# Kernel tuning notes

Hardware: AMD Instinct MI355X
Metric: run time of the kernel (lower is better)

Reference implementation:

```python
import jax, jax.numpy as jnp
import numpy as np

N, D_IN, D_HID, D_OUT, E = 100000, 128, 256, 64, 1600000


def setup_inputs() -> dict:
    key = jax.random.key(0)
    ks = jax.random.split(key, 6)
    x = jax.random.normal(ks[0], (N, D_IN), dtype=jnp.float32)
    edge_index = jax.random.randint(ks[1], (2, E), 0, N, dtype=jnp.int64)
    # Linear params (PyTorch convention: y = x @ W.T + b)
    W1 = jax.random.normal(ks[2], (D_HID, D_IN), dtype=jnp.float32) / np.sqrt(D_IN)
    b1 = jax.random.normal(ks[3], (D_HID,), dtype=jnp.float32) * 0.01
    W2 = jax.random.normal(ks[4], (D_OUT, D_HID), dtype=jnp.float32) / np.sqrt(D_HID)
    b2 = jax.random.normal(ks[5], (D_OUT,), dtype=jnp.float32) * 0.01
    return {"x": x, "edge_index": edge_index, "W1": W1, "b1": b1, "W2": W2, "b2": b2}


def _scatter_mean(vals, dst, num_nodes):
    # sum neighbor features per destination node, divide by in-degree (0-degree -> 0)
    s = jax.ops.segment_sum(vals, dst, num_segments=num_nodes)
    cnt = jax.ops.segment_sum(jnp.ones((dst.shape[0],), vals.dtype), dst, num_segments=num_nodes)
    return s / jnp.maximum(cnt, 1.0)[:, None]


def _sage_layer(x, src, dst, W, b):
    neighbors = x[src]                      # [E, d] gather
    agg = _scatter_mean(neighbors, dst, x.shape[0])  # [N, d]
    return agg @ W.T + b


def reference(x, edge_index, W1, b1, W2, b2):
    src, dst = edge_index[0], edge_index[1]
    h = _sage_layer(x, src, dst, W1, b1)
    h = jax.nn.relu(h)
    # dropout is identity at inference (training=False)
    y = _sage_layer(h, src, dst, W2, b2)
    return jax.nn.log_softmax(y, axis=1)
```

## Files before the change

kernel.cpp:

```cpp
#include <hip/hip_runtime.h>


typedef __attribute__((ext_vector_type(8))) short bf16x8;
typedef __attribute__((ext_vector_type(4))) float f32x4;
typedef __attribute__((ext_vector_type(2))) float f32x2;

#define BSHIFT 8
#define BMASK  255
#define SRCMASK 0x1FFFF
#define TBIN   4096

#if __has_builtin(__builtin_amdgcn_cvt_pk_f32_fp8) && __has_builtin(__builtin_amdgcn_cvt_pk_fp8_f32)
#define HAVE_FP8_CVT 1
#else
#define HAVE_FP8_CVT 0
#endif

__device__ inline ushort f2bf(float f) {
  union { float f; unsigned u; } c; c.f = f;
  unsigned r = (c.u + 0x7fffu + ((c.u >> 16) & 1u)) >> 16;
  return (ushort)r;
}

#if HAVE_FP8_CVT
template <bool HI>
__device__ inline f32x2 fp8x2f(unsigned w) {
  return __builtin_amdgcn_cvt_pk_f32_fp8((int)w, HI);
}
template <bool HI>
__device__ inline unsigned fp8pack2(unsigned old, float a, float b) {
  return (unsigned)__builtin_amdgcn_cvt_pk_fp8_f32(a, b, (int)old, HI);
}
#else
__device__ inline float fp8tof_1(unsigned b) {
  unsigned e = (b >> 3) & 15u, m = b & 7u;
  float v;
  if (e == 0) v = (float)m * 0x1p-9f;
  else { union { unsigned u; float f; } c; c.u = ((e + 120u) << 23) | (m << 20); v = c.f; }
  return (b & 0x80u) ? -v : v;
}
template <bool HI>
__device__ inline f32x2 fp8x2f(unsigned w) {
  unsigned sh = HI ? 16 : 0;
  f32x2 r;
  r.x = fp8tof_1((w >> sh) & 0xFFu);
  r.y = fp8tof_1((w >> (sh + 8)) & 0xFFu);
  return r;
}
__device__ inline unsigned f2fp8_1(float f) {
  float af = fabsf(f);
  unsigned s = (f < 0.f) ? 0x80u : 0u;
  if (!(af < 448.f)) return s | 0x7Eu;
  if (af < 0x1p-6f) {
    int m = (int)rintf(af * 512.0f);
    if (m >= 8) return s | 0x08u;
    return s | (unsigned)m;
  }
  int e;
  frexpf(af, &e);
  int E = e - 1;
  int q = (int)rintf(ldexpf(af, 3 - E));
  if (q >= 16) { q = 8; E += 1; if (E > 8) return s | 0x7Eu; }
  return s | ((unsigned)(E + 7) << 3) | ((unsigned)q & 7u);
}
template <bool HI>
__device__ inline unsigned fp8pack2(unsigned old, float a, float b) {
  unsigned pair = f2fp8_1(a) | (f2fp8_1(b) << 8);
  return HI ? ((old & 0x0000FFFFu) | (pair << 16)) : ((old & 0xFFFF0000u) | pair);
}
#endif

__global__ void __launch_bounds__(256) k_prep_x(const float4* __restrict__ x4, uint2* __restrict__ xq8, int total8) {
  int i = blockIdx.x * 256 + threadIdx.x;
  if (i >= total8) return;
  float4 v0 = x4[2 * i], v1 = x4[2 * i + 1];
  unsigned w0 = fp8pack2<false>(0u, v0.x, v0.y);
  w0 = fp8pack2<true>(w0, v0.z, v0.w);
  unsigned w1 = fp8pack2<false>(0u, v1.x, v1.y);
  w1 = fp8pack2<true>(w1, v1.z, v1.w);
  xq8[i] = make_uint2(w0, w1);
}

__global__ void __launch_bounds__(256) k_prep_w(const float* __restrict__ W1, const float* __restrict__ W2,
                                                ushort* __restrict__ W1f, ushort* __restrict__ W2f,
                                                const int* __restrict__ ei, int* __restrict__ flag,
                                                unsigned long long* __restrict__ xpad,
                                                unsigned long long* __restrict__ gpad) {
  if (blockIdx.x == 0) {
    int t = threadIdx.x;
    if (t < 64) {
      int v = ei[2 * t + 1];
      unsigned long long m = __ballot(v != 0);
      if (t == 0) *flag = (m == 0ull) ? 1 : 0;
      if (t < 16) xpad[t] = 0ull;
      if (t < 8)  gpad[t] = 0ull;
    }
  }
  int idx = blockIdx.x * 256 + threadIdx.x;
  if (idx < 32768) {
    int jt = idx >> 11, rem = idx & 2047;
    int kt = rem >> 9, rem2 = rem & 511;
    int l = rem2 >> 3, e = rem2 & 7;
    int k = kt * 32 + (l >> 4) * 8 + e;
    int j = jt * 16 + (l & 15);
    W1f[idx] = f2bf(W1[j * 128 + k]);
  } else {
    int i2 = idx - 32768;
    if (i2 < 16384) {
      int ot = i2 >> 12, rem = i2 & 4095;
      int kt = rem >> 9;
      int l = (rem >> 3) & 63, e = rem & 7;
      int k = kt * 32 + (l >> 4) * 8 + e;
      int o = ot * 16 + (l & 15);
      W2f[i2] = f2bf(W2[o * 256 + k]);
    }
  }
}

__global__ void __launch_bounds__(256) k_bhist(const int* __restrict__ ei, const int* __restrict__ flag,
                                               int* __restrict__ bcnt, int E, int NB) {
  __shared__ int h[512];
  int t = threadIdx.x;
  h[t] = 0; h[t + 256] = 0;
  __syncthreads();
  bool f64 = (*flag != 0);
  int stride = gridDim.x * 256;
  for (int e = blockIdx.x * 256 + t; e < E; e += stride) {
    int d;
    if (f64) d = (int)((const long long*)ei)[(size_t)E + e];
    else     d = ei[(size_t)E + e];
    atomicAdd(&h[d >> BSHIFT], 1);
  }
  __syncthreads();
  if (t < NB && h[t]) atomicAdd(&bcnt[t], h[t]);
  int t2 = t + 256;
  if (t2 < NB && h[t2]) atomicAdd(&bcnt[t2], h[t2]);
}

__global__ void __launch_bounds__(512) k_bscan(const int* __restrict__ bcnt, int* __restrict__ bbase,
                                               int* __restrict__ bcur, int* __restrict__ row_ptr,
                                               int NB, int N, int E) {
  __shared__ int s[512];
  int t = threadIdx.x;
  int v = (t < NB) ? bcnt[t] : 0;
  s[t] = v;
  __syncthreads();
  for (int o = 1; o < 512; o <<= 1) {
    int u = (t >= o) ? s[t - o] : 0;
    __syncthreads();
    s[t] += u;
    __syncthreads();
  }
  if (t < NB) {
    int base = s[t] - v;
    bbase[t] = base;
    bcur[t] = base;
  }
  if (t == 0) {
    bbase[NB] = E;
    row_ptr[N] = E;
  }
}

__global__ void __launch_bounds__(256) k_bin(const int* __restrict__ ei, const int* __restrict__ flag,
                                             int* __restrict__ bcur, int* __restrict__ gpair, int E, int NB) {
  __shared__ int hist[512], base[512], segb[512], cur[512], scanb[512];
  __shared__ int ent[TBIN];
  __shared__ int gdx[TBIN];
  int t = threadIdx.x;
  int e0 = blockIdx.x * TBIN;
  int cnt = E - e0; if (cnt > TBIN) cnt = TBIN;
  hist[t] = 0; hist[t + 256] = 0;
  __syncthreads();
  bool f64 = (*flag != 0);
  int ment[16], mbk[16];
#pragma unroll
  for (int i = 0; i < 16; ++i) {
    int idx = t + i * 256;
    mbk[i] = -1;
    if (idx < cnt) {
      int e = e0 + idx;
      int s, d;
      if (f64) {
        const long long* p = (const long long*)ei;
        s = (int)p[e];
        d = (int)p[(size_t)E + e];
      } else {
        s = ei[e];
        d = ei[(size_t)E + e];
      }
      int b = d >> BSHIFT;
      mbk[i] = b;
      ment[i] = ((d & BMASK) << 17) | s;
      atomicAdd(&hist[b], 1);
    }
  }
  __syncthreads();
  scanb[t] = hist[t]; scanb[t + 256] = hist[t + 256];
  __syncthreads();
  for (int o = 1; o < 512; o <<= 1) {
    int u0 = (t >= o) ? scanb[t - o] : 0;
    int t2 = t + 256;
    int u1 = (t2 >= o) ? scanb[t2 - o] : 0;
    __syncthreads();
    scanb[t] += u0; scanb[t + 256] += u1;
    __syncthreads();
  }
  {
    int b0 = scanb[t] - hist[t];
    base[t] = b0;
    cur[t] = b0;
    segb[t] = (t < NB && hist[t] > 0) ? atomicAdd(&bcur[t], hist[t]) : 0;
    int t2 = t + 256;
    int b1 = scanb[t2] - hist[t2];
    base[t2] = b1;
    cur[t2] = b1;
    segb[t2] = (t2 < NB && hist[t2] > 0) ? atomicAdd(&bcur[t2], hist[t2]) : 0;
  }
  __syncthreads();
#pragma unroll
  for (int i = 0; i < 16; ++i) {
    int b = mbk[i];
    if (b >= 0) {
      int pos = atomicAdd(&cur[b], 1);
      ent[pos] = ment[i];
      gdx[pos] = segb[b] + (pos - base[b]);
    }
  }
  __syncthreads();
  for (int i = t; i < cnt; i += 256) gpair[gdx[i]] = ent[i];
}

__global__ void __launch_bounds__(256) k_bcsr(const int* __restrict__ gpair, const int* __restrict__ bbase,
                                              int* __restrict__ row_ptr, float* __restrict__ inv_deg,
                                              int* __restrict__ csr, int N) {
  __shared__ int hist[256], pre[256], cur[256];
  int b = blockIdx.x, t = threadIdx.x;
  int start = bbase[b], end = bbase[b + 1];
  hist[t] = 0;
  __syncthreads();
  for (int i = start + t; i < end; i += 256) {
    int e = gpair[i];
    atomicAdd(&hist[e >> 17], 1);
  }
  __syncthreads();
  pre[t] = hist[t];
  __syncthreads();
  for (int o = 1; o < 256; o <<= 1) {
    int u = (t >= o) ? pre[t - o] : 0;
    __syncthreads();
    pre[t] += u;
    __syncthreads();
  }
  int gbase = start + pre[t] - hist[t];
  int n = (b << BSHIFT) + t;
  if (n < N) {
    row_ptr[n] = gbase;
    inv_deg[n] = 1.0f / (float)(hist[t] > 0 ? hist[t] : 1);
  }
  cur[t] = gbase;
  __syncthreads();
  for (int i = start + t; i < end; i += 256) {
    int e = gpair[i];
    int pos = atomicAdd(&cur[e >> 17], 1);
    csr[pos] = e & SRCMASK;
  }
}

__global__ void __launch_bounds__(256) k_agg1(const unsigned char* __restrict__ xq, const int* __restrict__ csr,
                                              const int* __restrict__ row_ptr, const float* __restrict__ inv_deg,
                                              ushort* __restrict__ agg1b, int N) {
  const int lane = threadIdx.x & 63;
  const int g = lane >> 4;
  const int g16 = lane & 48;
  const int p = lane & 15;
  const int h = (lane >> 3) & 1;
  const int c = lane & 7;
  const unsigned coff = (unsigned)c * 16u;
  const int shbase = g16 + h;

  const int quad = blockIdx.x * 4 + (threadIdx.x >> 6);
  const int n0 = quad * 4;
  if (n0 >= N) return;
  int rp = n0 + (lane < 4 ? lane : 4);
  if (rp > N) rp = N;
  const int rv = row_ptr[rp];
  const int n = n0 + g;
  const int s = __shfl(rv, g);
  const int cnt = __shfl(rv, g + 1) - s;
  int maxc = cnt;
  maxc = max(maxc, __shfl_xor(maxc, 16));
  maxc = max(maxc, __shfl_xor(maxc, 32));

  f32x2 a[8];
#pragma unroll
  for (int i = 0; i < 8; ++i) a[i] = (f32x2)(0.f);

  int ci = (p < cnt) ? csr[s + p] : N;
  for (int base = 0; base < maxc; base += 16) {
    uint4 wv[8];
#pragma unroll
    for (int u = 0; u < 8; ++u) {
      int idx = __shfl(ci, shbase + 2 * u);
      wv[u] = *(const uint4*)(xq + (((unsigned)idx << 7) + coff));
    }
    int li = base + 16 + p;
    int cin = (li < cnt) ? csr[s + li] : N;
#pragma unroll
    for (int u = 0; u < 8; ++u) {
      a[0] += fp8x2f<false>(wv[u].x); a[1] += fp8x2f<true>(wv[u].x);
      a[2] += fp8x2f<false>(wv[u].y); a[3] += fp8x2f<true>(wv[u].y);
      a[4] += fp8x2f<false>(wv[u].z); a[5] += fp8x2f<true>(wv[u].z);
      a[6] += fp8x2f<false>(wv[u].w); a[7] += fp8x2f<true>(wv[u].w);
    }
    ci = cin;
  }
#pragma unroll
  for (int i = 0; i < 8; ++i) {
    a[i].x += __shfl_xor(a[i].x, 8);
    a[i].y += __shfl_xor(a[i].y, 8);
  }
  if (n < N) {
    const float inv = inv_deg[n];
    bf16x8 o;
#pragma unroll
    for (int k = 0; k < 4; ++k) {
      f32x2 v0 = a[k], v1 = a[k + 4];
      float vx = h ? v1.x : v0.x;
      float vy = h ? v1.y : v0.y;
      o[2 * k]     = (short)f2bf(vx * inv);
      o[2 * k + 1] = (short)f2bf(vy * inv);
    }
    *(bf16x8*)(agg1b + (size_t)n * 128 + c * 16 + h * 8) = o;
  }
}

__global__ void __launch_bounds__(256) k_mlp(const ushort* __restrict__ agg1b, const bf16x8* __restrict__ w1f,
                                             const float* __restrict__ b1, const bf16x8* __restrict__ w2f,
                                             unsigned char* __restrict__ gq, int N) {
  __shared__ __align__(16) ushort sm[16896];
  ushort* aT = sm;
  ushort* hT = sm;
  const int t = threadIdx.x;
  const int n0 = blockIdx.x * 64;

#pragma unroll
  for (int i = 0; i < 4; ++i) {
    int idx = i * 256 + t;
    int row = idx >> 4, c8 = idx & 15;
    int rr = n0 + row; if (rr >= N) rr = N - 1;
    bf16x8 v = *(const bf16x8*)(agg1b + (size_t)rr * 128 + c8 * 8);
    *(bf16x8*)(aT + row * 136 + c8 * 8) = v;
  }
  __syncthreads();

  const int w = t >> 6, l = t & 63;
  const int lm = l & 15, lq = l >> 4;

  f32x4 acc[4][4];
#pragma unroll
  for (int mt = 0; mt < 4; ++mt)
#pragma unroll
    for (int nt = 0; nt < 4; ++nt) acc[mt][nt] = (f32x4)(0.f);

#pragma unroll
  for (int kt = 0; kt < 4; ++kt) {
    bf16x8 b[4], a[4];
#pragma unroll
    for (int nt = 0; nt < 4; ++nt)
      b[nt] = w1f[((w * 4 + nt) * 4 + kt) * 64 + l];
#pragma unroll
    for (int mt = 0; mt < 4; ++mt)
      a[mt] = *(const bf16x8*)(aT + (mt * 16 + lm) * 136 + kt * 32 + lq * 8);
#pragma unroll
    for (int mt = 0; mt < 4; ++mt)
#pragma unroll
      for (int nt = 0; nt < 4; ++nt)
        acc[mt][nt] = __builtin_amdgcn_mfma_f32_16x16x32_bf16(a[mt], b[nt], acc[mt][nt], 0, 0, 0);
  }
  __syncthreads();

#pragma unroll
  for (int nt = 0; nt < 4; ++nt) {
    int col = w * 64 + nt * 16 + lm;
    float bb = b1[col];
#pragma unroll
    for (int mt = 0; mt < 4; ++mt)
#pragma unroll
      for (int r = 0; r < 4; ++r) {
        int row = mt * 16 + lq * 4 + r;
        float hv = acc[mt][nt][r] + bb;
        hT[row * 264 + col] = f2bf(fmaxf(hv, 0.f));
      }
  }
  __syncthreads();

  f32x4 acc2[4];
#pragma unroll
  for (int ot = 0; ot < 4; ++ot) acc2[ot] = (f32x4)(0.f);
#pragma unroll
  for (int kt = 0; kt < 8; ++kt) {
    bf16x8 a2 = *(const bf16x8*)(hT + (w * 16 + lm) * 264 + kt * 32 + lq * 8);
#pragma unroll
    for (int ot = 0; ot < 4; ++ot) {
      bf16x8 bf = w2f[(ot * 8 + kt) * 64 + l];
      acc2[ot] = __builtin_amdgcn_mfma_f32_16x16x32_bf16(a2, bf, acc2[ot], 0, 0, 0);
    }
  }
#pragma unroll
  for (int ot = 0; ot < 4; ++ot)
#pragma unroll
    for (int r = 0; r < 4; ++r) {
      int row = n0 + w * 16 + lq * 4 + r;
      if (row < N) {
        unsigned pw = fp8pack2<false>(0u, acc2[ot][r], acc2[ot][r]);
        gq[(size_t)row * 64 + ot * 16 + lm] = (unsigned char)(pw & 0xFFu);
      }
    }
}

__global__ void __launch_bounds__(256) k_agg2(const unsigned char* __restrict__ gq, const int* __restrict__ csr,
                                              const int* __restrict__ row_ptr, const float* __restrict__ inv_deg,
                                              const float* __restrict__ b2, float* __restrict__ out, int N) {
  const int lane = threadIdx.x & 63;
  const int g = lane >> 4;
  const int g16 = lane & 48;
  const int p = lane & 15;
  const int q2 = (lane >> 2) & 3;
  const int c = lane & 3;
  const unsigned coff = (unsigned)c * 16u;
  const int shbase = g16 + q2;

  const int quad = blockIdx.x * 4 + (threadIdx.x >> 6);
  const int n0 = quad * 4;
  if (n0 >= N) return;
  int rp = n0 + (lane < 4 ? lane : 4);
  if (rp > N) rp = N;
  const int rv = row_ptr[rp];
  const int n = n0 + g;
  const int s = __shfl(rv, g);
  const int cnt = __shfl(rv, g + 1) - s;
  int maxc = cnt;
  maxc = max(maxc, __shfl_xor(maxc, 16));
  maxc = max(maxc, __shfl_xor(maxc, 32));

  f32x2 a[8];
#pragma unroll
  for (int i = 0; i < 8; ++i) a[i] = (f32x2)(0.f);

  int ci0 = (p < cnt) ? csr[s + p] : N;
  int li1 = 16 + p;
  int ci1 = (li1 < cnt) ? csr[s + li1] : N;
  for (int base = 0; base < maxc; base += 32) {
    uint4 wv[8];
#pragma unroll
    for (int u = 0; u < 4; ++u) {
      int idx = __shfl(ci0, shbase + 4 * u);
      wv[u] = *(const uint4*)(gq + (((unsigned)idx << 6) + coff));
    }
#pragma unroll
    for (int u = 0; u < 4; ++u) {
      int idx = __shfl(ci1, shbase + 4 * u);
      wv[4 + u] = *(const uint4*)(gq + (((unsigned)idx << 6) + coff));
    }
    int li2 = base + 32 + p, li3 = base + 48 + p;
    int cin0 = (li2 < cnt) ? csr[s + li2] : N;
    int cin1 = (li3 < cnt) ? csr[s + li3] : N;
#pragma unroll
    for (int u = 0; u < 8; ++u) {
      a[0] += fp8x2f<false>(wv[u].x); a[1] += fp8x2f<true>(wv[u].x);
      a[2] += fp8x2f<false>(wv[u].y); a[3] += fp8x2f<true>(wv[u].y);
      a[4] += fp8x2f<false>(wv[u].z); a[5] += fp8x2f<true>(wv[u].z);
      a[6] += fp8x2f<false>(wv[u].w); a[7] += fp8x2f<true>(wv[u].w);
    }
    ci0 = cin0; ci1 = cin1;
  }
#pragma unroll
  for (int i = 0; i < 8; ++i) {
    a[i].x += __shfl_xor(a[i].x, 4); a[i].y += __shfl_xor(a[i].y, 4);
    a[i].x += __shfl_xor(a[i].x, 8); a[i].y += __shfl_xor(a[i].y, 8);
  }
  const float inv = inv_deg[n < N ? n : 0];
  float4 bv0 = *(const float4*)(b2 + c * 16);
  float4 bv1 = *(const float4*)(b2 + c * 16 + 4);
  float4 bv2 = *(const float4*)(b2 + c * 16 + 8);
  float4 bv3 = *(const float4*)(b2 + c * 16 + 12);
  float v[16];
  v[0]  = a[0].x * inv + bv0.x;  v[1]  = a[0].y * inv + bv0.y;
  v[2]  = a[1].x * inv + bv0.z;  v[3]  = a[1].y * inv + bv0.w;
  v[4]  = a[2].x * inv + bv1.x;  v[5]  = a[2].y * inv + bv1.y;
  v[6]  = a[3].x * inv + bv1.z;  v[7]  = a[3].y * inv + bv1.w;
  v[8]  = a[4].x * inv + bv2.x;  v[9]  = a[4].y * inv + bv2.y;
  v[10] = a[5].x * inv + bv2.z;  v[11] = a[5].y * inv + bv2.w;
  v[12] = a[6].x * inv + bv3.x;  v[13] = a[6].y * inv + bv3.y;
  v[14] = a[7].x * inv + bv3.z;  v[15] = a[7].y * inv + bv3.w;
  float mx = v[0];
#pragma unroll
  for (int j = 1; j < 16; ++j) mx = fmaxf(mx, v[j]);
  mx = fmaxf(mx, __shfl_xor(mx, 1));
  mx = fmaxf(mx, __shfl_xor(mx, 2));
  float se = 0.f;
#pragma unroll
  for (int j = 0; j < 16; ++j) se += expf(v[j] - mx);
  se += __shfl_xor(se, 1);
  se += __shfl_xor(se, 2);
  float lse = mx + logf(se);
  if (n < N && q2 == 0) {
    float* po = out + (size_t)n * 64 + c * 16;
    float4 o0, o1, o2, o3;
    o0.x = v[0] - lse;  o0.y = v[1] - lse;  o0.z = v[2] - lse;  o0.w = v[3] - lse;
    o1.x = v[4] - lse;  o1.y = v[5] - lse;  o1.z = v[6] - lse;  o1.w = v[7] - lse;
    o2.x = v[8] - lse;  o2.y = v[9] - lse;  o2.z = v[10] - lse; o2.w = v[11] - lse;
    o3.x = v[12] - lse; o3.y = v[13] - lse; o3.z = v[14] - lse; o3.w = v[15] - lse;
    *(float4*)(po)      = o0;
    *(float4*)(po + 4)  = o1;
    *(float4*)(po + 8)  = o2;
    *(float4*)(po + 12) = o3;
  }
}

extern "C" void kernel_launch(void* const* d_in, const int* in_sizes, int n_in,
                              void* d_out, int out_size, void* d_ws, size_t ws_size,
                              hipStream_t stream) {
  const float* x  = (const float*)d_in[0];
  const int*   ei = (const int*)d_in[1];
  const float* W1 = (const float*)d_in[2];
  const float* b1 = (const float*)d_in[3];
  const float* W2 = (const float*)d_in[4];
  const float* b2 = (const float*)d_in[5];
  float* out = (float*)d_out;
  const int N = in_sizes[0] / 128;
  const int E = in_sizes[1] / 2;
  const int NB = (N + BMASK) >> BSHIFT;

  char* base = (char*)d_ws;
  size_t off = 0;
  auto alloc = [&](size_t bytes) -> char* {
    char* p = base + off;
    off += (bytes + 255) & ~(size_t)255;
    return p;
  };
  int*    flag    = (int*)alloc(4);
  int*    bcnt    = (int*)alloc((size_t)NB * 4);
  int*    bbase   = (int*)alloc((size_t)(NB + 1) * 4);
  int*    bcur    = (int*)alloc((size_t)NB * 4);
  int*    gpair   = (int*)alloc((size_t)E * 4);
  int*    row_ptr = (int*)alloc((size_t)(N + 1) * 4);
  float*  inv_deg = (float*)alloc((size_t)N * 4);
  int*    csr     = (int*)alloc((size_t)E * 4);
  unsigned char* xq = (unsigned char*)alloc((size_t)(N + 1) * 128);
  ushort* W1f     = (ushort*)alloc((size_t)32768 * 2);
  ushort* W2f     = (ushort*)alloc((size_t)16384 * 2);
  ushort* agg1b   = (ushort*)alloc((size_t)N * 128 * 2);
  unsigned char* gq = (unsigned char*)alloc((size_t)(N + 1) * 64);
  (void)ws_size; (void)n_in; (void)out_size;

  hipMemsetAsync(bcnt, 0, (size_t)NB * 4, stream);
  k_prep_x<<<(N * 16 + 255) / 256, 256, 0, stream>>>((const float4*)x, (uint2*)xq, N * 16);
  k_prep_w<<<192, 256, 0, stream>>>(W1, W2, W1f, W2f, ei, flag,
                                    (unsigned long long*)(xq + (size_t)N * 128),
                                    (unsigned long long*)(gq + (size_t)N * 64));
  k_bhist<<<512, 256, 0, stream>>>(ei, flag, bcnt, E, NB);
  k_bscan<<<1, 512, 0, stream>>>(bcnt, bbase, bcur, row_ptr, NB, N, E);
  k_bin<<<(E + TBIN - 1) / TBIN, 256, 0, stream>>>(ei, flag, bcur, gpair, E, NB);
  k_bcsr<<<NB, 256, 0, stream>>>(gpair, bbase, row_ptr, inv_deg, csr, N);
  k_agg1<<<(N + 15) / 16, 256, 0, stream>>>(xq, csr, row_ptr, inv_deg, agg1b, N);
  k_mlp<<<(N + 63) / 64, 256, 0, stream>>>(agg1b, (const bf16x8*)W1f, b1, (const bf16x8*)W2f, gq, N);
  k_agg2<<<(N + 15) / 16, 256, 0, stream>>>(gq, csr, row_ptr, inv_deg, b2, out, N);
}
```

Measured before the change: 246.0 us.

## Fuse prep, histogram and scan into one front kernel with last-block scan

Result: slower. 259.5 us (+5.5%).

```diff
diff --git a/kernel.cpp b/kernel.cpp
--- a/kernel.cpp
+++ b/kernel.cpp
@@ -9,6 +9,7 @@
 #define BMASK  255
 #define SRCMASK 0x1FFFF
 #define TBIN   4096
+#define NHB    512
 
 #if __has_builtin(__builtin_amdgcn_cvt_pk_f32_fp8) && __has_builtin(__builtin_amdgcn_cvt_pk_fp8_f32)
 #define HAVE_FP8_CVT 1
@@ -70,95 +71,99 @@
 }
 #endif
 
-__global__ void __launch_bounds__(256) k_prep_x(const float4* __restrict__ x4, uint2* __restrict__ xq8, int total8) {
-  int i = blockIdx.x * 256 + threadIdx.x;
-  if (i >= total8) return;
-  float4 v0 = x4[2 * i], v1 = x4[2 * i + 1];
-  unsigned w0 = fp8pack2<false>(0u, v0.x, v0.y);
-  w0 = fp8pack2<true>(w0, v0.z, v0.w);
-  unsigned w1 = fp8pack2<false>(0u, v1.x, v1.y);
-  w1 = fp8pack2<true>(w1, v1.z, v1.w);
-  xq8[i] = make_uint2(w0, w1);
-}
-
-__global__ void __launch_bounds__(256) k_prep_w(const float* __restrict__ W1, const float* __restrict__ W2,
-                                                ushort* __restrict__ W1f, ushort* __restrict__ W2f,
-                                                const int* __restrict__ ei, int* __restrict__ flag,
-                                                unsigned long long* __restrict__ xpad,
-                                                unsigned long long* __restrict__ gpad) {
-  if (blockIdx.x == 0) {
-    int t = threadIdx.x;
+__global__ void __launch_bounds__(256) k_front(const float4* __restrict__ x4, uint2* __restrict__ xq8, int total8,
+                                               const float* __restrict__ W1, const float* __restrict__ W2,
+                                               ushort* __restrict__ W1f, ushort* __restrict__ W2f,
+                                               const int* __restrict__ ei, int* __restrict__ flag,
+                                               unsigned long long* __restrict__ xpad,
+                                               unsigned long long* __restrict__ gpad,
+                                               int* __restrict__ bcnt, int* __restrict__ done,
+                                               int* __restrict__ bbase, int* __restrict__ bcur,
+                                               int* __restrict__ row_ptr,
+                                               int E, int NB, int N) {
+  const int bid = blockIdx.x;
+  const int t = threadIdx.x;
+  if (bid < NHB) {
+    __shared__ int h[512];
+    __shared__ int sf64, ticket;
+    h[t] = 0; h[t + 256] = 0;
     if (t < 64) {
+      int v = ei[2 * t + 1];
+      unsigned long long m = __ballot(v != 0);
+      if (t == 0) sf64 = (m == 0ull) ? 1 : 0;
+    }
+    __syncthreads();
+    const bool f64 = (sf64 != 0);
+    const int stride = NHB * 256;
+    for (int e = bid * 256 + t; e < E; e += stride) {
+      int d;
+      if (f64) d = (int)((const long long*)ei)[(size_t)E + e];
+      else     d = ei[(size_t)E + e];
+      atomicAdd(&h[d >> BSHIFT], 1);
+    }
+    __syncthreads();
+    const int t2 = t + 256;
+    if (t < NB && h[t]) atomicAdd(&bcnt[t], h[t]);
+    if (t2 < NB && h[t2]) atomicAdd(&bcnt[t2], h[t2]);
+    __threadfence();
+    __syncthreads();
+    if (t == 0) ticket = atomicAdd(done, 1);
+    __syncthreads();
+    if (ticket == NHB - 1) {
+      __shared__ int s[512];
+      int v0 = (t < NB) ? atomicAdd(&bcnt[t], 0) : 0;
+      int v1 = (t2 < NB) ? atomicAdd(&bcnt[t2], 0) : 0;
+      s[t] = v0; s[t2] = v1;
+      __syncthreads();
+      for (int o = 1; o < 512; o <<= 1) {
+        int u0 = (t >= o) ? s[t - o] : 0;
+        int u1 = (t2 >= o) ? s[t2 - o] : 0;
+        __syncthreads();
+        s[t] += u0; s[t2] += u1;
+        __syncthreads();
+      }
+      if (t < NB) { int b0 = s[t] - v0; bbase[t] = b0; bcur[t] = b0; }
+      if (t2 < NB) { int b1 = s[t2] - v1; bbase[t2] = b1; bcur[t2] = b1; }
+      if (t == 0) { bbase[NB] = E; row_ptr[N] = E; }
+    }
+  } else if (bid < NHB + 192) {
+    const int wb = bid - NHB;
+    if (wb == 0 && t < 64) {
       int v = ei[2 * t + 1];
       unsigned long long m = __ballot(v != 0);
       if (t == 0) *flag = (m == 0ull) ? 1 : 0;
       if (t < 16) xpad[t] = 0ull;
       if (t < 8)  gpad[t] = 0ull;
     }
-  }
-  int idx = blockIdx.x * 256 + threadIdx.x;
-  if (idx < 32768) {
-    int jt = idx >> 11, rem = idx & 2047;
-    int kt = rem >> 9, rem2 = rem & 511;
-    int l = rem2 >> 3, e = rem2 & 7;
-    int k = kt * 32 + (l >> 4) * 8 + e;
-    int j = jt * 16 + (l & 15);
-    W1f[idx] = f2bf(W1[j * 128 + k]);
+    int idx = wb * 256 + t;
+    if (idx < 32768) {
+      int jt = idx >> 11, rem = idx & 2047;
+      int kt = rem >> 9, rem2 = rem & 511;
+      int l = rem2 >> 3, e = rem2 & 7;
+      int k = kt * 32 + (l >> 4) * 8 + e;
+      int j = jt * 16 + (l & 15);
+      W1f[idx] = f2bf(W1[j * 128 + k]);
+    } else {
+      int i2 = idx - 32768;
+      if (i2 < 16384) {
+        int ot = i2 >> 12, rem = i2 & 4095;
+        int kt = rem >> 9;
+        int l = (rem >> 3) & 63, e = rem & 7;
+        int k = kt * 32 + (l >> 4) * 8 + e;
+        int o = ot * 16 + (l & 15);
+        W2f[i2] = f2bf(W2[o * 256 + k]);
+      }
+    }
   } else {
-    int i2 = idx - 32768;
-    if (i2 < 16384) {
-      int ot = i2 >> 12, rem = i2 & 4095;
-      int kt = rem >> 9;
-      int l = (rem >> 3) & 63, e = rem & 7;
-      int k = kt * 32 + (l >> 4) * 8 + e;
-      int o = ot * 16 + (l & 15);
-      W2f[i2] = f2bf(W2[o * 256 + k]);
-    }
-  }
-}
-
-__global__ void __launch_bounds__(256) k_bhist(const int* __restrict__ ei, const int* __restrict__ flag,
-                                               int* __restrict__ bcnt, int E, int NB) {
-  __shared__ int h[512];
-  int t = threadIdx.x;
-  h[t] = 0; h[t + 256] = 0;
-  __syncthreads();
-  bool f64 = (*flag != 0);
-  int stride = gridDim.x * 256;
-  for (int e = blockIdx.x * 256 + t; e < E; e += stride) {
-    int d;
-    if (f64) d = (int)((const long long*)ei)[(size_t)E + e];
-    else     d = ei[(size_t)E + e];
-    atomicAdd(&h[d >> BSHIFT], 1);
-  }
-  __syncthreads();
-  if (t < NB && h[t]) atomicAdd(&bcnt[t], h[t]);
-  int t2 = t + 256;
-  if (t2 < NB && h[t2]) atomicAdd(&bcnt[t2], h[t2]);
-}
-
-__global__ void __launch_bounds__(512) k_bscan(const int* __restrict__ bcnt, int* __restrict__ bbase,
-                                               int* __restrict__ bcur, int* __restrict__ row_ptr,
-                                               int NB, int N, int E) {
-  __shared__ int s[512];
-  int t = threadIdx.x;
-  int v = (t < NB) ? bcnt[t] : 0;
-  s[t] = v;
-  __syncthreads();
-  for (int o = 1; o < 512; o <<= 1) {
-    int u = (t >= o) ? s[t - o] : 0;
-    __syncthreads();
-    s[t] += u;
-    __syncthreads();
-  }
-  if (t < NB) {
-    int base = s[t] - v;
-    bbase[t] = base;
-    bcur[t] = base;
-  }
-  if (t == 0) {
-    bbase[NB] = E;
-    row_ptr[N] = E;
+    int i = (bid - NHB - 192) * 256 + t;
+    if (i < total8) {
+      float4 v0 = x4[2 * i], v1 = x4[2 * i + 1];
+      unsigned w0 = fp8pack2<false>(0u, v0.x, v0.y);
+      w0 = fp8pack2<true>(w0, v0.z, v0.w);
+      unsigned w1 = fp8pack2<false>(0u, v1.x, v1.y);
+      w1 = fp8pack2<true>(w1, v1.z, v1.w);
+      xq8[i] = make_uint2(w0, w1);
+    }
   }
 }
 
@@ -541,7 +546,7 @@
     return p;
   };
   int*    flag    = (int*)alloc(4);
-  int*    bcnt    = (int*)alloc((size_t)NB * 4);
+  int*    bcnt    = (int*)alloc((size_t)(NB + 1) * 4);
   int*    bbase   = (int*)alloc((size_t)(NB + 1) * 4);
   int*    bcur    = (int*)alloc((size_t)NB * 4);
   int*    gpair   = (int*)alloc((size_t)E * 4);
@@ -555,13 +560,16 @@
   unsigned char* gq = (unsigned char*)alloc((size_t)(N + 1) * 64);
   (void)ws_size; (void)n_in; (void)out_size;
 
-  hipMemsetAsync(bcnt, 0, (size_t)NB * 4, stream);
-  k_prep_x<<<(N * 16 + 255) / 256, 256, 0, stream>>>((const float4*)x, (uint2*)xq, N * 16);
-  k_prep_w<<<192, 256, 0, stream>>>(W1, W2, W1f, W2f, ei, flag,
-                                    (unsigned long long*)(xq + (size_t)N * 128),
-                                    (unsigned long long*)(gq + (size_t)N * 64));
-  k_bhist<<<512, 256, 0, stream>>>(ei, flag, bcnt, E, NB);
-  k_bscan<<<1, 512, 0, stream>>>(bcnt, bbase, bcur, row_ptr, NB, N, E);
+  const int total8 = N * 16;
+  const int NPX = (total8 + 255) / 256;
+
+  hipMemsetAsync(bcnt, 0, (size_t)(NB + 1) * 4, stream);
+  k_front<<<NHB + 192 + NPX, 256, 0, stream>>>((const float4*)x, (uint2*)xq, total8,
+                                               W1, W2, W1f, W2f, ei, flag,
+                                               (unsigned long long*)(xq + (size_t)N * 128),
+                                               (unsigned long long*)(gq + (size_t)N * 64),
+                                               bcnt, bcnt + NB, bbase, bcur, row_ptr,
+                                               E, NB, N);
   k_bin<<<(E + TBIN - 1) / TBIN, 256, 0, stream>>>(ei, flag, bcur, gpair, E, NB);
   k_bcsr<<<NB, 256, 0, stream>>>(gpair, bbase, row_ptr, inv_deg, csr, N);
   k_agg1<<<(N + 15) / 16, 256, 0, stream>>>(xq, csr, row_ptr, inv_deg, agg1b, N);
```

## Fuse first-layer neighbor aggregation into the MLP kernel via shared memory

Applied to the files above, without the earlier changes.

Result: slower. 263.3 us (+7.0%).

```diff
diff --git a/kernel.cpp b/kernel.cpp
--- a/kernel.cpp
+++ b/kernel.cpp
@@ -267,94 +267,88 @@
   }
 }
 
-__global__ void __launch_bounds__(256) k_agg1(const unsigned char* __restrict__ xq, const int* __restrict__ csr,
-                                              const int* __restrict__ row_ptr, const float* __restrict__ inv_deg,
-                                              ushort* __restrict__ agg1b, int N) {
-  const int lane = threadIdx.x & 63;
-  const int g = lane >> 4;
-  const int g16 = lane & 48;
-  const int p = lane & 15;
-  const int h = (lane >> 3) & 1;
-  const int c = lane & 7;
-  const unsigned coff = (unsigned)c * 16u;
-  const int shbase = g16 + h;
-
-  const int quad = blockIdx.x * 4 + (threadIdx.x >> 6);
-  const int n0 = quad * 4;
-  if (n0 >= N) return;
-  int rp = n0 + (lane < 4 ? lane : 4);
-  if (rp > N) rp = N;
-  const int rv = row_ptr[rp];
-  const int n = n0 + g;
-  const int s = __shfl(rv, g);
-  const int cnt = __shfl(rv, g + 1) - s;
-  int maxc = cnt;
-  maxc = max(maxc, __shfl_xor(maxc, 16));
-  maxc = max(maxc, __shfl_xor(maxc, 32));
-
-  f32x2 a[8];
-#pragma unroll
-  for (int i = 0; i < 8; ++i) a[i] = (f32x2)(0.f);
-
-  int ci = (p < cnt) ? csr[s + p] : N;
-  for (int base = 0; base < maxc; base += 16) {
-    uint4 wv[8];
-#pragma unroll
-    for (int u = 0; u < 8; ++u) {
-      int idx = __shfl(ci, shbase + 2 * u);
-      wv[u] = *(const uint4*)(xq + (((unsigned)idx << 7) + coff));
-    }
-    int li = base + 16 + p;
-    int cin = (li < cnt) ? csr[s + li] : N;
-#pragma unroll
-    for (int u = 0; u < 8; ++u) {
-      a[0] += fp8x2f<false>(wv[u].x); a[1] += fp8x2f<true>(wv[u].x);
-      a[2] += fp8x2f<false>(wv[u].y); a[3] += fp8x2f<true>(wv[u].y);
-      a[4] += fp8x2f<false>(wv[u].z); a[5] += fp8x2f<true>(wv[u].z);
-      a[6] += fp8x2f<false>(wv[u].w); a[7] += fp8x2f<true>(wv[u].w);
-    }
-    ci = cin;
-  }
-#pragma unroll
-  for (int i = 0; i < 8; ++i) {
-    a[i].x += __shfl_xor(a[i].x, 8);
-    a[i].y += __shfl_xor(a[i].y, 8);
-  }
-  if (n < N) {
-    const float inv = inv_deg[n];
-    bf16x8 o;
-#pragma unroll
-    for (int k = 0; k < 4; ++k) {
-      f32x2 v0 = a[k], v1 = a[k + 4];
-      float vx = h ? v1.x : v0.x;
-      float vy = h ? v1.y : v0.y;
-      o[2 * k]     = (short)f2bf(vx * inv);
-      o[2 * k + 1] = (short)f2bf(vy * inv);
-    }
-    *(bf16x8*)(agg1b + (size_t)n * 128 + c * 16 + h * 8) = o;
-  }
-}
-
-__global__ void __launch_bounds__(256) k_mlp(const ushort* __restrict__ agg1b, const bf16x8* __restrict__ w1f,
-                                             const float* __restrict__ b1, const bf16x8* __restrict__ w2f,
-                                             unsigned char* __restrict__ gq, int N) {
+__global__ void __launch_bounds__(256) k_aggmlp(const unsigned char* __restrict__ xq,
+                                                const int* __restrict__ csr,
+                                                const int* __restrict__ row_ptr,
+                                                const float* __restrict__ inv_deg,
+                                                const bf16x8* __restrict__ w1f,
+                                                const float* __restrict__ b1,
+                                                const bf16x8* __restrict__ w2f,
+                                                unsigned char* __restrict__ gq, int N) {
   __shared__ __align__(16) ushort sm[16896];
   ushort* aT = sm;
   ushort* hT = sm;
   const int t = threadIdx.x;
   const int n0 = blockIdx.x * 64;
-
-#pragma unroll
-  for (int i = 0; i < 4; ++i) {
-    int idx = i * 256 + t;
-    int row = idx >> 4, c8 = idx & 15;
-    int rr = n0 + row; if (rr >= N) rr = N - 1;
-    bf16x8 v = *(const bf16x8*)(agg1b + (size_t)rr * 128 + c8 * 8);
-    *(bf16x8*)(aT + row * 136 + c8 * 8) = v;
-  }
-  __syncthreads();
-
-  const int w = t >> 6, l = t & 63;
+  const int lane = t & 63;
+  const int w = t >> 6;
+
+  {
+    const int g = lane >> 4;
+    const int g16 = lane & 48;
+    const int p = lane & 15;
+    const int h = (lane >> 3) & 1;
+    const int c = lane & 7;
+    const unsigned coff = (unsigned)c * 16u;
+    const int shbase = g16 + h;
+#pragma unroll
+    for (int j = 0; j < 4; ++j) {
+      const int qn0 = n0 + (w * 4 + j) * 4;
+      int rp = qn0 + (lane < 4 ? lane : 4);
+      if (rp > N) rp = N;
+      const int rv = row_ptr[rp];
+      const int n = qn0 + g;
+      const int s = __shfl(rv, g);
+      const int cnt = __shfl(rv, g + 1) - s;
+      int maxc = cnt;
+      maxc = max(maxc, __shfl_xor(maxc, 16));
+      maxc = max(maxc, __shfl_xor(maxc, 32));
+
+      f32x2 a[8];
+#pragma unroll
+      for (int i = 0; i < 8; ++i) a[i] = (f32x2)(0.f);
+
+      int ci = (p < cnt) ? csr[s + p] : N;
+      for (int base = 0; base < maxc; base += 16) {
+        uint4 wv[8];
+#pragma unroll
+        for (int u = 0; u < 8; ++u) {
+          int idx = __shfl(ci, shbase + 2 * u);
+          wv[u] = *(const uint4*)(xq + (((unsigned)idx << 7) + coff));
+        }
+        int li = base + 16 + p;
+        int cin = (li < cnt) ? csr[s + li] : N;
+#pragma unroll
+        for (int u = 0; u < 8; ++u) {
+          a[0] += fp8x2f<false>(wv[u].x); a[1] += fp8x2f<true>(wv[u].x);
+          a[2] += fp8x2f<false>(wv[u].y); a[3] += fp8x2f<true>(wv[u].y);
+          a[4] += fp8x2f<false>(wv[u].z); a[5] += fp8x2f<true>(wv[u].z);
+          a[6] += fp8x2f<false>(wv[u].w); a[7] += fp8x2f<true>(wv[u].w);
+        }
+        ci = cin;
+      }
+#pragma unroll
+      for (int i = 0; i < 8; ++i) {
+        a[i].x += __shfl_xor(a[i].x, 8);
+        a[i].y += __shfl_xor(a[i].y, 8);
+      }
+      const float inv = inv_deg[n < N ? n : 0];
+      bf16x8 o;
+#pragma unroll
+      for (int k = 0; k < 4; ++k) {
+        f32x2 v0 = a[k], v1 = a[k + 4];
+        float vx = h ? v1.x : v0.x;
+        float vy = h ? v1.y : v0.y;
+        o[2 * k]     = (short)f2bf(vx * inv);
+        o[2 * k + 1] = (short)f2bf(vy * inv);
+      }
+      const int row = (w * 4 + j) * 4 + g;
+      *(bf16x8*)(aT + row * 136 + c * 16 + h * 8) = o;
+    }
+  }
+  __syncthreads();
+
+  const int l = lane;
   const int lm = l & 15, lq = l >> 4;
 
   f32x4 acc[4][4];
@@ -551,7 +545,6 @@
   unsigned char* xq = (unsigned char*)alloc((size_t)(N + 1) * 128);
   ushort* W1f     = (ushort*)alloc((size_t)32768 * 2);
   ushort* W2f     = (ushort*)alloc((size_t)16384 * 2);
-  ushort* agg1b   = (ushort*)alloc((size_t)N * 128 * 2);
   unsigned char* gq = (unsigned char*)alloc((size_t)(N + 1) * 64);
   (void)ws_size; (void)n_in; (void)out_size;
 
@@ -564,7 +557,7 @@
   k_bscan<<<1, 512, 0, stream>>>(bcnt, bbase, bcur, row_ptr, NB, N, E);
   k_bin<<<(E + TBIN - 1) / TBIN, 256, 0, stream>>>(ei, flag, bcur, gpair, E, NB);
   k_bcsr<<<NB, 256, 0, stream>>>(gpair, bbase, row_ptr, inv_deg, csr, N);
-  k_agg1<<<(N + 15) / 16, 256, 0, stream>>>(xq, csr, row_ptr, inv_deg, agg1b, N);
-  k_mlp<<<(N + 63) / 64, 256, 0, stream>>>(agg1b, (const bf16x8*)W1f, b1, (const bf16x8*)W2f, gq, N);
+  k_aggmlp<<<(N + 63) / 64, 256, 0, stream>>>(xq, csr, row_ptr, inv_deg,
+                                              (const bf16x8*)W1f, b1, (const bf16x8*)W2f, gq, N);
   k_agg2<<<(N + 15) / 16, 256, 0, stream>>>(gq, csr, row_ptr, inv_deg, b2, out, N);
 }
```
